# Kernel optimization log

Hardware: AMD Instinct MI355X
Metric: run time of the kernel (lower is better)

Reference implementation:

```python
import jax, jax.numpy as jnp
import numpy as np

B, T, D, H = 2, 2048, 1024, 16  # batch, seq_len, d_model (d_in==d_out), num_heads
HD = D // H  # head_dim = 64


def setup_inputs() -> dict:
    key = jax.random.key(0)
    ks = jax.random.split(key, 6)
    s = 1.0 / np.sqrt(D)
    return {
        "x": jax.random.normal(ks[0], (B, T, D), dtype=jnp.float32),
        "wq": jax.random.normal(ks[1], (D, D), dtype=jnp.float32) * s,
        "wk": jax.random.normal(ks[2], (D, D), dtype=jnp.float32) * s,
        "wv": jax.random.normal(ks[3], (D, D), dtype=jnp.float32) * s,
        "wo": jax.random.normal(ks[4], (D, D), dtype=jnp.float32) * s,
        "bo": jax.random.normal(ks[5], (D,), dtype=jnp.float32) * 0.01,
    }


def reference(x, wq, wk, wv, wo, bo):
    b, t, d = x.shape
    # projections (qkv_bias=False), split heads: [b, h, t, hd]
    q = (x @ wq).reshape(b, t, H, HD).transpose(0, 2, 1, 3)
    k = (x @ wk).reshape(b, t, H, HD).transpose(0, 2, 1, 3)
    v = (x @ wv).reshape(b, t, H, HD).transpose(0, 2, 1, 3)
    # causal attention scores [b, h, t, t]
    scores = jnp.einsum("bhqd,bhkd->bhqk", q, k) / jnp.sqrt(jnp.float32(HD))
    causal = jnp.tril(jnp.ones((t, t), dtype=bool))
    scores = jnp.where(causal[None, None, :, :], scores, -jnp.inf)
    attn = jax.nn.softmax(scores, axis=-1)  # dropout p=0.0 -> identity
    ctx = jnp.einsum("bhqk,bhkd->bhqd", attn, v)  # [b, h, t, hd]
    ctx = ctx.transpose(0, 2, 1, 3).reshape(b, t, d)  # merge heads
    return ctx @ wo + bo
```

## Files before the change

### kernel.cpp

```cpp
#include <hip/hip_runtime.h>
#include <hip/hip_bf16.h>
#include <stdint.h>

#define B_  2
#define T_  2048
#define D_  1024
#define H_  16
#define HD_ 64

typedef __bf16 bf16x8 __attribute__((ext_vector_type(8)));
typedef __bf16 bf16x4 __attribute__((ext_vector_type(4)));
typedef float  f32x4  __attribute__((ext_vector_type(4)));

__device__ __forceinline__ void async_copy16(const void* g, void* l) {
  __builtin_amdgcn_global_load_lds((__attribute__((address_space(1))) void*)(g),
                                   (__attribute__((address_space(3))) void*)(l),
                                   16, 0, 0);
}

__global__ void prep_kernel(const float* __restrict__ x,
                            const float* __restrict__ wq, const float* __restrict__ wk,
                            const float* __restrict__ wv, const float* __restrict__ wo,
                            __bf16* __restrict__ xc,
                            __bf16* __restrict__ wqkv_t, __bf16* __restrict__ wo_t) {
  const int id  = blockIdx.x;
  const int tid = threadIdx.x;
  if (id < 4096) {
    __shared__ __bf16 tile[32][33];
    const int z   = id >> 10;
    const int rem = id & 1023;
    const int n0 = (rem & 31) * 32, k0 = (rem >> 5) * 32;
    const int tx = tid & 31, ty = tid >> 5;
    const float* src = (z == 0) ? wq : (z == 1) ? wk : (z == 2) ? wv : wo;
    __bf16* dst = (z < 3) ? (wqkv_t + (size_t)z * 1024 * 1024) : wo_t;
#pragma unroll
    for (int i = 0; i < 4; ++i)
      tile[ty + 8 * i][tx] = (__bf16)src[(size_t)(k0 + ty + 8 * i) * 1024 + n0 + tx];
    __syncthreads();
#pragma unroll
    for (int i = 0; i < 4; ++i)
      dst[(size_t)(n0 + ty + 8 * i) * 1024 + k0 + tx] = tile[tx][ty + 8 * i];
  } else {
    const int i0 = ((id - 4096) * 256 + tid) * 4;
    bf16x4 v;
#pragma unroll
    for (int k = 0; k < 4; ++k) v[k] = (__bf16)x[i0 + k];
    *(bf16x4*)(xc + i0) = v;
  }
}

template <int MODE>
__launch_bounds__(256)
__global__ void gemm128_kernel(const __bf16* __restrict__ A, const __bf16* __restrict__ Bt, int K,
                               __bf16* __restrict__ q_b, __bf16* __restrict__ k_b,
                               __bf16* __restrict__ vt_b,
                               const float* __restrict__ bo, float* __restrict__ outp) {
  __shared__ __align__(16) __bf16 As[128 * 64];
  __shared__ __align__(16) __bf16 Bs[128 * 64];
  const int tid  = threadIdx.x;
  const int w    = tid >> 6, lane = tid & 63;
  const int quad = lane >> 4, lr = lane & 15;
  const int tm = blockIdx.y * 128, tn = blockIdx.x * 128;
  const int wm = (w >> 1) * 64, wn = (w & 1) * 64;
  const int lrow   = lane >> 3;
  const int gchunk = (lane & 7) ^ lrow;

  f32x4 acc[4][4] = {};

  for (int k0 = 0; k0 < K; k0 += 64) {
#pragma unroll
    for (int c = 0; c < 4; ++c) {
      const int chunk = w * 4 + c;
      const int row   = chunk * 8 + lrow;
      async_copy16(A  + (size_t)(tm + row) * K + k0 + gchunk * 8, As + chunk * 512);
      async_copy16(Bt + (size_t)(tn + row) * K + k0 + gchunk * 8, Bs + chunk * 512);
    }
    __syncthreads();
#pragma unroll
    for (int ks = 0; ks < 2; ++ks) {
      bf16x8 af[4], bfr[4];
#pragma unroll
      for (int mi = 0; mi < 4; ++mi) {
        const int row = wm + mi * 16 + lr;
        const int ch  = (ks * 4 + quad) ^ (row & 7);
        af[mi] = *(const bf16x8*)(As + row * 64 + ch * 8);
      }
#pragma unroll
      for (int ni = 0; ni < 4; ++ni) {
        const int row = wn + ni * 16 + lr;
        const int ch  = (ks * 4 + quad) ^ (row & 7);
        bfr[ni] = *(const bf16x8*)(Bs + row * 64 + ch * 8);
      }
#pragma unroll
      for (int mi = 0; mi < 4; ++mi)
#pragma unroll
        for (int ni = 0; ni < 4; ++ni)
          acc[mi][ni] = __builtin_amdgcn_mfma_f32_16x16x32_bf16(af[mi], bfr[ni], acc[mi][ni], 0, 0, 0);
    }
    __syncthreads();
  }

  if (MODE == 0) {
#pragma unroll
    for (int mi = 0; mi < 4; ++mi) {
      const int mrow0 = tm + wm + mi * 16 + quad * 4;
      const int b  = mrow0 >> 11;
      const int t0 = mrow0 & 2047;
#pragma unroll
      for (int ni = 0; ni < 4; ++ni) {
        const int ncol = tn + wn + ni * 16 + lr;
        const int mat  = ncol >> 10;
        const int nn   = ncol & 1023;
        const int h = nn >> 6, hd = nn & 63;
        if (mat == 0) {
#pragma unroll
          for (int r = 0; r < 4; ++r)
            q_b[((size_t)((b * H_ + h) * T_ + t0 + r)) * HD_ + hd] =
                (__bf16)(acc[mi][ni][r] * 0.125f);
        } else if (mat == 1) {
#pragma unroll
          for (int r = 0; r < 4; ++r)
            k_b[((size_t)((b * H_ + h) * T_ + t0 + r)) * HD_ + hd] =
                (__bf16)(acc[mi][ni][r]);
        } else {
          bf16x4 pk;
#pragma unroll
          for (int r = 0; r < 4; ++r) pk[r] = (__bf16)(acc[mi][ni][r]);
          *(bf16x4*)(vt_b + ((size_t)(b * H_ + h) * HD_ + hd) * T_ + t0) = pk;
        }
      }
    }
  } else {
#pragma unroll
    for (int mi = 0; mi < 4; ++mi) {
      const int m0 = tm + wm + mi * 16 + quad * 4;
#pragma unroll
      for (int ni = 0; ni < 4; ++ni) {
        const int n = tn + wn + ni * 16 + lr;
        const float bias = bo[n];
#pragma unroll
        for (int r = 0; r < 4; ++r)
          outp[(size_t)(m0 + r) * D_ + n] = acc[mi][ni][r] + bias;
      }
    }
  }
}

__launch_bounds__(256)
__global__ void attn_kernel(const __bf16* __restrict__ q_b, const __bf16* __restrict__ k_b,
                            const __bf16* __restrict__ vt_b, __bf16* __restrict__ ctx) {
  __shared__ __align__(16) __bf16 sK[64 * 64];
  __shared__ __align__(16) __bf16 sV[64 * 64];
  __shared__ __align__(16) __bf16 sP[4][2][16][72];
  const int tid  = threadIdx.x;
  const int w    = tid >> 6, lane = tid & 63;
  const int quad = lane >> 4, lr = lane & 15;
  const int id = blockIdx.x;
  const int bh  = (id & 7) * 4 + ((id >> 3) & 3);
  const int t0i = (id >> 5) & 7;
  const int rnd = id >> 8;
  const int tq  = (3 - rnd) * 8 + ((rnd & 1) ? t0i : (7 - t0i));
  const __bf16* qh = q_b  + (size_t)bh * T_ * HD_;
  const __bf16* kh = k_b  + (size_t)bh * T_ * HD_;
  const __bf16* vh = vt_b + (size_t)bh * HD_ * T_;
  const int b = bh >> 4, h = bh & 15;

  const int r0 = tid >> 3, r1 = (tid + 256) >> 3;
  const int g0 = tid & 7;

  const int q0 = tq * 64 + w * 16;
  const int nj = tq + 1;

  bf16x8 qf[2];
#pragma unroll
  for (int ks = 0; ks < 2; ++ks)
    qf[ks] = *(const bf16x8*)(qh + (size_t)(q0 + lr) * HD_ + ks * 32 + quad * 8);

  f32x4 o[4] = {};
  float lsum[4] = {0.f, 0.f, 0.f, 0.f};

  bf16x8 kr0 = *(const bf16x8*)(kh + (size_t)r0 * HD_ + g0 * 8);
  bf16x8 kr1 = *(const bf16x8*)(kh + (size_t)r1 * HD_ + g0 * 8);
  bf16x8 vr0 = *(const bf16x8*)(vh + (size_t)r0 * T_ + g0 * 8);
  bf16x8 vr1 = *(const bf16x8*)(vh + (size_t)r1 * T_ + g0 * 8);

  for (int j = 0; j < nj; ++j) {
    const int j0 = j * 64;
    const int pb = j & 1;
    __syncthreads();
    *(bf16x8*)(sK + r0 * 64 + (g0 ^ (r0 & 7)) * 8) = kr0;
    *(bf16x8*)(sK + r1 * 64 + (g0 ^ (r1 & 7)) * 8) = kr1;
    *(bf16x8*)(sV + r0 * 64 + (g0 ^ (r0 & 7)) * 8) = vr0;
    *(bf16x8*)(sV + r1 * 64 + (g0 ^ (r1 & 7)) * 8) = vr1;
    __syncthreads();
    if (j + 1 < nj) {
      const int jn = j0 + 64;
      kr0 = *(const bf16x8*)(kh + (size_t)(jn + r0) * HD_ + g0 * 8);
      kr1 = *(const bf16x8*)(kh + (size_t)(jn + r1) * HD_ + g0 * 8);
      vr0 = *(const bf16x8*)(vh + (size_t)r0 * T_ + jn + g0 * 8);
      vr1 = *(const bf16x8*)(vh + (size_t)r1 * T_ + jn + g0 * 8);
    }
    f32x4 s[4] = {};
    __builtin_amdgcn_s_setprio(1);
#pragma unroll
    for (int ni = 0; ni < 4; ++ni) {
      const int row = ni * 16 + lr;
#pragma unroll
      for (int ks = 0; ks < 2; ++ks) {
        const int ch = (ks * 4 + quad) ^ (row & 7);
        bf16x8 kf = *(const bf16x8*)(sK + row * 64 + ch * 8);
        s[ni] = __builtin_amdgcn_mfma_f32_16x16x32_bf16(qf[ks], kf, s[ni], 0, 0, 0);
      }
    }
    __builtin_amdgcn_s_setprio(0);
    if (j0 + 63 > q0) {
#pragma unroll
      for (int ni = 0; ni < 4; ++ni) {
        const int col = j0 + ni * 16 + lr;
#pragma unroll
        for (int r = 0; r < 4; ++r) {
          const int row = q0 + quad * 4 + r;
          if (col > row) s[ni][r] = -3.0e38f;
        }
      }
    }
#pragma unroll
    for (int ni = 0; ni < 4; ++ni)
#pragma unroll
      for (int r = 0; r < 4; ++r)
        s[ni][r] = __expf(s[ni][r]);
#pragma unroll
    for (int r = 0; r < 4; ++r)
      lsum[r] += (s[0][r] + s[1][r]) + (s[2][r] + s[3][r]);
#pragma unroll
    for (int ni = 0; ni < 4; ++ni)
#pragma unroll
      for (int r = 0; r < 4; ++r)
        sP[w][pb][quad * 4 + r][ni * 16 + lr] = (__bf16)s[ni][r];
    asm volatile("s_waitcnt lgkmcnt(0)" ::: "memory");
    bf16x8 pf[2];
#pragma unroll
    for (int ks = 0; ks < 2; ++ks)
      pf[ks] = *(const bf16x8*)(&sP[w][pb][lr][ks * 32 + quad * 8]);
    __builtin_amdgcn_s_setprio(1);
#pragma unroll
    for (int ni = 0; ni < 4; ++ni) {
      const int row = ni * 16 + lr;
#pragma unroll
      for (int ks = 0; ks < 2; ++ks) {
        const int ch = (ks * 4 + quad) ^ (row & 7);
        bf16x8 vf = *(const bf16x8*)(sV + row * 64 + ch * 8);
        o[ni] = __builtin_amdgcn_mfma_f32_16x16x32_bf16(pf[ks], vf, o[ni], 0, 0, 0);
      }
    }
    __builtin_amdgcn_s_setprio(0);
  }
#pragma unroll
  for (int off = 1; off <= 8; off <<= 1)
#pragma unroll
    for (int r = 0; r < 4; ++r)
      lsum[r] += __shfl_xor(lsum[r], off, 16);
#pragma unroll
  for (int r = 0; r < 4; ++r) {
    const float inv = 1.0f / lsum[r];
    const int t = q0 + quad * 4 + r;
#pragma unroll
    for (int ni = 0; ni < 4; ++ni)
      ctx[((size_t)(b * T_ + t)) * D_ + h * HD_ + ni * 16 + lr] =
          (__bf16)(o[ni][r] * inv);
  }
}

extern "C" void kernel_launch(void* const* d_in, const int* in_sizes, int n_in,
                              void* d_out, int out_size, void* d_ws, size_t ws_size,
                              hipStream_t stream) {
  (void)in_sizes; (void)n_in; (void)out_size; (void)ws_size;
  const float* x  = (const float*)d_in[0];
  const float* wq = (const float*)d_in[1];
  const float* wk = (const float*)d_in[2];
  const float* wv = (const float*)d_in[3];
  const float* wo = (const float*)d_in[4];
  const float* bo = (const float*)d_in[5];
  float* outp = (float*)d_out;

  char* ws = (char*)d_ws;
  __bf16* ctx    = (__bf16*)(ws + 0);
  __bf16* wqkv_t = (__bf16*)(ws + 0);
  __bf16* wo_t   = (__bf16*)(ws + 8388608);
  __bf16* q_b    = (__bf16*)(ws + 10485760);
  __bf16* k_b    = (__bf16*)(ws + 18874368);
  __bf16* vt_b   = (__bf16*)(ws + 27262976);
  __bf16* xc     = (__bf16*)(ws + 35651584);

  prep_kernel<<<8192, 256, 0, stream>>>(x, wq, wk, wv, wo, xc, wqkv_t, wo_t);
  gemm128_kernel<0><<<dim3(24, 32), 256, 0, stream>>>(xc, wqkv_t, 1024, q_b, k_b, vt_b, nullptr, nullptr);
  attn_kernel<<<1024, 256, 0, stream>>>(q_b, k_b, vt_b, ctx);
  gemm128_kernel<1><<<dim3(8, 32), 256, 0, stream>>>(ctx, wo_t, 1024, nullptr, nullptr, nullptr, bo, outp);
}
```

Measured before the change: 181.0 us.

## Split QK^T across warps by key columns and compute row sums via MFMA

Each warp now keeps all 64 query rows' Q fragments in registers and computes scores for its own 16-key slice, so each warp loads only two K fragments from LDS instead of eight. The probability tile is shared across the block in LDS, and a block barrier is added before each warp reads its 16 query rows for the PV product. Softmax row sums come from an extra MFMA against a ones vector, which removes the scalar adds and the final shuffle reduction. The launch bound asks for 3 waves per SIMD. The costs are more Q registers and an extra __syncthreads per key tile.

After: 176.9 us. 2.3% less time.

```diff
diff --git a/kernel.cpp b/kernel.cpp
--- a/kernel.cpp
+++ b/kernel.cpp
@@ -146,12 +146,12 @@
   }
 }
 
-__launch_bounds__(256)
+__launch_bounds__(256, 3)
 __global__ void attn_kernel(const __bf16* __restrict__ q_b, const __bf16* __restrict__ k_b,
                             const __bf16* __restrict__ vt_b, __bf16* __restrict__ ctx) {
   __shared__ __align__(16) __bf16 sK[64 * 64];
   __shared__ __align__(16) __bf16 sV[64 * 64];
-  __shared__ __align__(16) __bf16 sP[4][2][16][72];
+  __shared__ __align__(16) __bf16 sP[2][64][72];
   const int tid  = threadIdx.x;
   const int w    = tid >> 6, lane = tid & 63;
   const int quad = lane >> 4, lr = lane & 15;
@@ -168,16 +168,23 @@
   const int r0 = tid >> 3, r1 = (tid + 256) >> 3;
   const int g0 = tid & 7;
 
-  const int q0 = tq * 64 + w * 16;
+  const int q0 = tq * 64;
   const int nj = tq + 1;
-
-  bf16x8 qf[2];
-#pragma unroll
-  for (int ks = 0; ks < 2; ++ks)
-    qf[ks] = *(const bf16x8*)(qh + (size_t)(q0 + lr) * HD_ + ks * 32 + quad * 8);
+  const int w16 = w * 16;
+
+  bf16x8 qf[4][2];
+#pragma unroll
+  for (int qs = 0; qs < 4; ++qs)
+#pragma unroll
+    for (int ks = 0; ks < 2; ++ks)
+      qf[qs][ks] = *(const bf16x8*)(qh + (size_t)(q0 + qs * 16 + lr) * HD_ + ks * 32 + quad * 8);
+
+  bf16x8 onesf;
+#pragma unroll
+  for (int j = 0; j < 8; ++j) onesf[j] = (__bf16)1.0f;
 
   f32x4 o[4] = {};
-  float lsum[4] = {0.f, 0.f, 0.f, 0.f};
+  f32x4 ls = {};
 
   bf16x8 kr0 = *(const bf16x8*)(kh + (size_t)r0 * HD_ + g0 * 8);
   bf16x8 kr1 = *(const bf16x8*)(kh + (size_t)r1 * HD_ + g0 * 8);
@@ -200,48 +207,43 @@
       vr0 = *(const bf16x8*)(vh + (size_t)r0 * T_ + jn + g0 * 8);
       vr1 = *(const bf16x8*)(vh + (size_t)r1 * T_ + jn + g0 * 8);
     }
+    const int krow = w16 + lr;
+    bf16x8 kf[2];
+    kf[0] = *(const bf16x8*)(sK + krow * 64 + ((quad) ^ (krow & 7)) * 8);
+    kf[1] = *(const bf16x8*)(sK + krow * 64 + ((4 + quad) ^ (krow & 7)) * 8);
     f32x4 s[4] = {};
     __builtin_amdgcn_s_setprio(1);
 #pragma unroll
-    for (int ni = 0; ni < 4; ++ni) {
-      const int row = ni * 16 + lr;
-#pragma unroll
-      for (int ks = 0; ks < 2; ++ks) {
-        const int ch = (ks * 4 + quad) ^ (row & 7);
-        bf16x8 kf = *(const bf16x8*)(sK + row * 64 + ch * 8);
-        s[ni] = __builtin_amdgcn_mfma_f32_16x16x32_bf16(qf[ks], kf, s[ni], 0, 0, 0);
-      }
+    for (int qs = 0; qs < 4; ++qs) {
+      s[qs] = __builtin_amdgcn_mfma_f32_16x16x32_bf16(qf[qs][0], kf[0], s[qs], 0, 0, 0);
+      s[qs] = __builtin_amdgcn_mfma_f32_16x16x32_bf16(qf[qs][1], kf[1], s[qs], 0, 0, 0);
     }
     __builtin_amdgcn_s_setprio(0);
     if (j0 + 63 > q0) {
-#pragma unroll
-      for (int ni = 0; ni < 4; ++ni) {
-        const int col = j0 + ni * 16 + lr;
+      const int col = j0 + w16 + lr;
+#pragma unroll
+      for (int qs = 0; qs < 4; ++qs)
 #pragma unroll
         for (int r = 0; r < 4; ++r) {
-          const int row = q0 + quad * 4 + r;
-          if (col > row) s[ni][r] = -3.0e38f;
+          const int row = q0 + qs * 16 + quad * 4 + r;
+          if (col > row) s[qs][r] = -3.0e38f;
         }
-      }
-    }
-#pragma unroll
-    for (int ni = 0; ni < 4; ++ni)
+    }
+#pragma unroll
+    for (int qs = 0; qs < 4; ++qs)
 #pragma unroll
       for (int r = 0; r < 4; ++r)
-        s[ni][r] = __expf(s[ni][r]);
-#pragma unroll
-    for (int r = 0; r < 4; ++r)
-      lsum[r] += (s[0][r] + s[1][r]) + (s[2][r] + s[3][r]);
-#pragma unroll
-    for (int ni = 0; ni < 4; ++ni)
+        s[qs][r] = __expf(s[qs][r]);
+#pragma unroll
+    for (int qs = 0; qs < 4; ++qs)
 #pragma unroll
       for (int r = 0; r < 4; ++r)
-        sP[w][pb][quad * 4 + r][ni * 16 + lr] = (__bf16)s[ni][r];
-    asm volatile("s_waitcnt lgkmcnt(0)" ::: "memory");
+        sP[pb][qs * 16 + quad * 4 + r][w16 + lr] = (__bf16)s[qs][r];
+    __syncthreads();
     bf16x8 pf[2];
 #pragma unroll
     for (int ks = 0; ks < 2; ++ks)
-      pf[ks] = *(const bf16x8*)(&sP[w][pb][lr][ks * 32 + quad * 8]);
+      pf[ks] = *(const bf16x8*)(&sP[pb][w16 + lr][ks * 32 + quad * 8]);
     __builtin_amdgcn_s_setprio(1);
 #pragma unroll
     for (int ni = 0; ni < 4; ++ni) {
@@ -253,17 +255,14 @@
         o[ni] = __builtin_amdgcn_mfma_f32_16x16x32_bf16(pf[ks], vf, o[ni], 0, 0, 0);
       }
     }
+    ls = __builtin_amdgcn_mfma_f32_16x16x32_bf16(pf[0], onesf, ls, 0, 0, 0);
+    ls = __builtin_amdgcn_mfma_f32_16x16x32_bf16(pf[1], onesf, ls, 0, 0, 0);
     __builtin_amdgcn_s_setprio(0);
   }
 #pragma unroll
-  for (int off = 1; off <= 8; off <<= 1)
-#pragma unroll
-    for (int r = 0; r < 4; ++r)
-      lsum[r] += __shfl_xor(lsum[r], off, 16);
-#pragma unroll
   for (int r = 0; r < 4; ++r) {
-    const float inv = 1.0f / lsum[r];
-    const int t = q0 + quad * 4 + r;
+    const float inv = 1.0f / ls[r];
+    const int t = q0 + w16 + quad * 4 + r;
 #pragma unroll
     for (int ni = 0; ni < 4; ++ni)
       ctx[((size_t)(b * T_ + t)) * D_ + h * HD_ + ni * 16 + lr] =
```
